# Performance work log

Measured on AMD Instinct MI355X. Metric: run time of the kernel, lower is better.

The kernel has to match this reference:

```python
import jax, jax.numpy as jnp
import numpy as np

D_MODEL = 2048
NUM_HEADS = 16
D_K = D_MODEL // NUM_HEADS  # 128
MAX_SEQ_LEN = 4096
THETA = 10000.0
BATCH = 2
SEQ = 2048


def _trunc_normal(key, shape, std):
    # approximate trunc_normal_(mean=0, std, a=-3std, b=3std)
    return jnp.clip(jax.random.normal(key, shape) * std, -3 * std, 3 * std)


def setup_inputs() -> dict:
    key = jax.random.key(0)
    k0, k1, k2, k3, k4 = jax.random.split(key, 5)
    std = 2.0 / (D_MODEL + D_MODEL) ** 0.5
    in_features = jax.random.normal(k0, (BATCH, SEQ, D_MODEL), dtype=jnp.float32)
    token_positions = jnp.arange(SEQ, dtype=jnp.int64 if jax.config.jax_enable_x64 else jnp.int32)
    wq = _trunc_normal(k1, (D_MODEL, D_MODEL), std)
    wk = _trunc_normal(k2, (D_MODEL, D_MODEL), std)
    wv = _trunc_normal(k3, (D_MODEL, D_MODEL), std)
    wo = _trunc_normal(k4, (D_MODEL, D_MODEL), std)
    return {"in_features": in_features, "token_positions": token_positions,
            "wq": wq, "wk": wk, "wv": wv, "wo": wo}


def _rope(x, token_positions):
    # x: [b, h, s, d_k]; token_positions: [s]
    freqs = 1.0 / THETA ** (jnp.arange(0, D_K, 2, dtype=jnp.float32) / D_K)  # [d_k/2]
    angles = token_positions.astype(jnp.float32)[:, None] * freqs[None, :]   # [s, d_k/2]
    sin = jnp.sin(angles)
    cos = jnp.cos(angles)
    x1 = x[..., ::2]
    x2 = x[..., 1::2]
    rot = jnp.stack([x1 * cos - x2 * sin, x1 * sin + x2 * cos], axis=-1)  # [b,h,s,d_k/2,2]
    return rot.reshape(x.shape)


def reference(in_features, token_positions, wq, wk, wv, wo):
    b, s, _ = in_features.shape
    # projections: weight is [d_out, d_in]
    q = jnp.einsum('oi,bsi->bso', wq, in_features)
    k = jnp.einsum('oi,bsi->bso', wk, in_features)
    v = jnp.einsum('oi,bsi->bso', wv, in_features)
    # split heads: [b, s, h*d] -> [b, h, s, d]
    def split(t):
        return t.reshape(b, s, NUM_HEADS, D_K).transpose(0, 2, 1, 3)
    q, k, v = split(q), split(k), split(v)
    q = _rope(q, token_positions)
    k = _rope(k, token_positions)
    scores = jnp.einsum('bhqd,bhkd->bhqk', q, k) / jnp.sqrt(jnp.float32(D_K))
    causal = jnp.tril(jnp.ones((s, s), dtype=bool))
    scores = jnp.where(causal, scores, -jnp.inf)
    attn = jax.nn.softmax(scores, axis=-1)
    out = jnp.einsum('bhqk,bhkd->bhqd', attn, v)
    out = out.transpose(0, 2, 1, 3).reshape(b, s, D_MODEL)
    return jnp.einsum('oi,bsi->bso', wo, out)
```

## Files before the change

kernel.cpp:

```cpp
#include <hip/hip_runtime.h>
#include <cstdint>

typedef unsigned short u16;
typedef __attribute__((ext_vector_type(8))) short short8;
typedef __attribute__((ext_vector_type(4))) float f32x4;
typedef __attribute__((ext_vector_type(16))) float f32x16;
typedef __attribute__((ext_vector_type(2))) unsigned int uint2v;

#define D_MODEL 2048
#define NHEAD   16
#define DK      128
#define SEQQ    2048
#define BATCH   2
#define MTOT    (BATCH*SEQQ)

#define FENCE() asm volatile("" ::: "memory")
#define BARRIER() do { FENCE(); __builtin_amdgcn_s_barrier(); FENCE(); } while (0)

__device__ __forceinline__ u16 f2b(float f) {
  union { float f; uint32_t u; } c; c.f = f;
  uint32_t u = c.u;
  u += 0x7fffu + ((u >> 16) & 1u);
  return (u16)(u >> 16);
}
__device__ __forceinline__ float b2f(u16 h) {
  union { uint32_t u; float f; } c; c.u = ((uint32_t)h) << 16;
  return c.f;
}

__device__ __forceinline__ void gload_lds16(const void* g, void* l) {
  __builtin_amdgcn_global_load_lds(
      (const __attribute__((address_space(1))) void*)(uintptr_t)g,
      (__attribute__((address_space(3))) void*)(uint32_t)(uintptr_t)l,
      16, 0, 0);
}

__global__ __launch_bounds__(256) void cvt_all(const float* __restrict__ x,
                                               const float* __restrict__ wq,
                                               const float* __restrict__ wk,
                                               const float* __restrict__ wv,
                                               const float* __restrict__ wo,
                                               u16* __restrict__ Xb,
                                               u16* __restrict__ Wqkv,
                                               u16* __restrict__ Wob) {
  int i = blockIdx.x * 256 + threadIdx.x;
  const float* src; u16* dst; int j;
  if (i < 2097152) {
    src = x; dst = Xb; j = i;
  } else {
    int t = i - 2097152;
    int w = t >> 20; j = t & 1048575;
    src = (w == 0) ? wq : (w == 1) ? wk : (w == 2) ? wv : wo;
    dst = (w < 3) ? (Wqkv + (size_t)w * 4194304) : Wob;
  }
  float4 v = ((const float4*)src)[j];
  union { u16 s[4]; uint64_t q; } o;
  o.s[0] = f2b(v.x); o.s[1] = f2b(v.y); o.s[2] = f2b(v.z); o.s[3] = f2b(v.w);
  ((uint64_t*)dst)[j] = o.q;
}

template<int MF, int NF, int MODE, int MAP>
__global__ __launch_bounds__(512) void gemmT(const u16* __restrict__ A,
                                             const u16* __restrict__ B,
                                             u16* __restrict__ Cq, u16* __restrict__ Ck,
                                             u16* __restrict__ Vt, float* __restrict__ Cf,
                                             int nbm, int cpx) {
  constexpr int BM = MF * 32;
  constexpr int BN = NF * 64;
  constexpr int AG = BM / 64;
  constexpr int BG = NF;
  __shared__ __align__(16) u16 As[2][BM * 64];
  __shared__ __align__(16) u16 Bs[2][BN * 64];
  const int tid = threadIdx.x;
  const int wave = tid >> 6, lane = tid & 63;
  const int l15 = lane & 15, l4 = lane >> 4;
  const int wr = wave >> 2, wc = wave & 3;
  int bm, bn;
  if (MAP == 1) {
    const int xcd = (int)blockIdx.x & 7;
    const int loc = (int)blockIdx.x >> 3;
    bm = ((loc >> 5) << 3) + (loc & 7);
    bn = xcd * 4 + ((loc >> 3) & 3);
  } else {
    const int wg = ((int)blockIdx.x & 7) * cpx + ((int)blockIdx.x >> 3);
    bm = wg % nbm; bn = wg / nbm;
  }
  const int row0 = bm * BM, col0 = bn * BN;

  const u16* asrc[AG]; const u16* bsrc[BG];
  {
    const int r = tid >> 3, c8 = tid & 7;
#pragma unroll
    for (int g = 0; g < AG; ++g) {
      int row = g * 64 + r;
      asrc[g] = A + (size_t)(row0 + row) * 2048 + ((c8 ^ (row & 7)) << 3);
    }
#pragma unroll
    for (int g = 0; g < BG; ++g) {
      int row = g * 64 + r;
      bsrc[g] = B + (size_t)(col0 + row) * 2048 + ((c8 ^ (row & 7)) << 3);
    }
  }
  const int ldst = tid * 8;

  int aoff[MF][2], boff[NF][2];
#pragma unroll
  for (int m = 0; m < MF; ++m) {
    int row = wr * (MF * 16) + m * 16 + l15;
#pragma unroll
    for (int ks = 0; ks < 2; ++ks)
      aoff[m][ks] = row * 64 + (((ks * 4 + l4) ^ (l15 & 7)) << 3);
  }
#pragma unroll
  for (int n = 0; n < NF; ++n) {
    int row = wc * (NF * 16) + n * 16 + l15;
#pragma unroll
    for (int ks = 0; ks < 2; ++ks)
      boff[n][ks] = row * 64 + (((ks * 4 + l4) ^ (l15 & 7)) << 3);
  }

  f32x4 acc[MF][NF] = {};

#pragma unroll
  for (int g = 0; g < AG; ++g) gload_lds16(asrc[g], &As[0][g * 4096 + ldst]);
#pragma unroll
  for (int g = 0; g < BG; ++g) gload_lds16(bsrc[g], &Bs[0][g * 4096 + ldst]);

  for (int t = 0; t < 32; ++t) {
    const int buf = t & 1;
    __syncthreads();
    if (t + 1 < 32) {
#pragma unroll
      for (int g = 0; g < AG; ++g) gload_lds16(asrc[g] + ((t + 1) << 6), &As[buf ^ 1][g * 4096 + ldst]);
#pragma unroll
      for (int g = 0; g < BG; ++g) gload_lds16(bsrc[g] + ((t + 1) << 6), &Bs[buf ^ 1][g * 4096 + ldst]);
    }
    short8 bfr[NF][2], afr[MF][2];
#pragma unroll
    for (int n = 0; n < NF; ++n)
#pragma unroll
      for (int ks = 0; ks < 2; ++ks)
        bfr[n][ks] = *(const short8*)&Bs[buf][boff[n][ks]];
#pragma unroll
    for (int m = 0; m < MF; ++m)
#pragma unroll
      for (int ks = 0; ks < 2; ++ks)
        afr[m][ks] = *(const short8*)&As[buf][aoff[m][ks]];
    __builtin_amdgcn_s_setprio(1);
#pragma unroll
    for (int ks = 0; ks < 2; ++ks)
#pragma unroll
      for (int n = 0; n < NF; ++n)
#pragma unroll
        for (int m = 0; m < MF; ++m)
          acc[m][n] = __builtin_amdgcn_mfma_f32_16x16x32_bf16(afr[m][ks], bfr[n][ks], acc[m][n], 0, 0, 0);
    __builtin_amdgcn_s_setprio(0);
  }

#pragma unroll
  for (int m = 0; m < MF; ++m) {
    const int row = row0 + wr * (MF * 16) + m * 16 + l4 * 4;
#pragma unroll
    for (int n = 0; n < NF; ++n) {
      const int col = col0 + wc * (NF * 16) + n * 16 + l15;
      if (MODE == 1) {
#pragma unroll
        for (int r = 0; r < 4; ++r)
          Cf[(size_t)(row + r) * 2048 + col] = acc[m][n][r];
      } else {
        const int region = col >> 11;
        const int col2 = col & 2047;
        if (region < 2) {
          u16* Cx = region ? Ck : Cq;
#pragma unroll
          for (int r = 0; r < 4; ++r)
            Cx[(size_t)(row + r) * 2048 + col2] = f2b(acc[m][n][r]);
        } else {
          union { u16 h4[4]; uint64_t q; } pk;
#pragma unroll
          for (int r = 0; r < 4; ++r) pk.h4[r] = f2b(acc[m][n][r]);
          const int bb = row >> 11, ss = row & 2047;
          const int hh = col2 >> 7, dd = col2 & 127;
          *(uint64_t*)&Vt[((size_t)((bb << 4) + hh) * 128 + dd) * 2048 + ss] = pk.q;
        }
      }
    }
  }
}

__global__ __launch_bounds__(256) void rope_qk(u16* __restrict__ Qb, u16* __restrict__ Kb,
                                               const int* __restrict__ pos) {
  int p = blockIdx.x * 256 + threadIdx.x;
  u16* X = (p >> 22) ? Kb : Qb;
  int pp = p & 4194303;
  int m = pp >> 10, j2 = pp & 1023;
  int h = j2 >> 6, j = j2 & 63;
  int s = m & (SEQQ - 1);
  float fp = (float)pos[s];
  float freq = exp2f((float)j * -0.20762050593046014f);
  float ang = fp * freq;
  float sn, cs;
  sincosf(ang, &sn, &cs);
  u16* px = X + (size_t)m * D_MODEL + h * DK + 2 * j;
  uint32_t pair = *(uint32_t*)px;
  float x1 = b2f((u16)(pair & 0xffff)), x2 = b2f((u16)(pair >> 16));
  u16 r1 = f2b(x1 * cs - x2 * sn);
  u16 r2 = f2b(x1 * sn + x2 * cs);
  *(uint32_t*)px = (uint32_t)r1 | ((uint32_t)r2 << 16);
}

__global__ __launch_bounds__(256) void attn_fwd(const u16* __restrict__ Q,
                                                const u16* __restrict__ Kg,
                                                const u16* __restrict__ Vt,
                                                u16* __restrict__ O) {
  __shared__ __align__(16) u16 Klds[2][64 * 128];
  __shared__ __align__(16) u16 Vlds[2][128 * 64];
  const int tid = threadIdx.x, wave = tid >> 6, lane = tid & 63;
  const int l31 = lane & 31, l5 = lane >> 5;
  const int bh = blockIdx.x;
  const int bxr = 15 - (int)blockIdx.y;
  const int b = bh >> 4, h = bh & 15;
  const int q0 = bxr * 128, qw = q0 + wave * 32;
  const float qscale = 0.1275174470974136f;

  short8 bq[8];
  {
    const u16* Qp = Q + (size_t)(b * SEQQ + qw + l31) * D_MODEL + h * DK + l5 * 8;
#pragma unroll
    for (int dt = 0; dt < 8; ++dt) {
      short8 raw = *(const short8*)(Qp + dt * 16);
#pragma unroll
      for (int j = 0; j < 8; ++j) raw[j] = (short)f2b(b2f((u16)raw[j]) * qscale);
      bq[dt] = raw;
    }
  }
  asm volatile("s_waitcnt vmcnt(0)" ::: "memory");

  f32x16 facc[4] = {};
  float mrun = -1e30f, lpart = 0.f;

  const u16* Kbase = Kg + (size_t)b * SEQQ * D_MODEL + h * DK;
  const u16* Vbase = Vt + (size_t)bh * DK * SEQQ;
  const u16* ksrc[4]; const u16* vsrc[4];
#pragma unroll
  for (int g = 0; g < 4; ++g) {
    int kr = g * 16 + (tid >> 4);
    int kc = ((tid & 15) * 8) ^ ((kr & 7) << 3);
    ksrc[g] = Kbase + (size_t)kr * D_MODEL + kc;
    int vr = g * 32 + (tid >> 3);
    int vc = ((tid & 7) * 8) ^ ((vr & 7) << 3);
    vsrc[g] = Vbase + (size_t)vr * SEQQ + vc;
  }
  const int dstoff = tid * 8;
  const int nkt = 2 * (bxr + 1);

#pragma unroll
  for (int g = 0; g < 4; ++g) { gload_lds16(ksrc[g], &Klds[0][g * 2048 + dstoff]); ksrc[g] += (size_t)64 * D_MODEL; }
#pragma unroll
  for (int g = 0; g < 4; ++g) { gload_lds16(vsrc[g], &Vlds[0][g * 2048 + dstoff]); vsrc[g] += 64; }

  for (int kt = 0; kt < nkt; ++kt) {
    const int k0 = kt * 64, cur = kt & 1;
    asm volatile("s_waitcnt vmcnt(0)" ::: "memory");
    BARRIER();
    if (kt + 1 < nkt) {
#pragma unroll
      for (int g = 0; g < 4; ++g) { gload_lds16(ksrc[g], &Klds[cur ^ 1][g * 2048 + dstoff]); ksrc[g] += (size_t)64 * D_MODEL; }
#pragma unroll
      for (int g = 0; g < 4; ++g) { gload_lds16(vsrc[g], &Vlds[cur ^ 1][g * 2048 + dstoff]); vsrc[g] += 64; }
    }
    if (k0 > qw + 31) continue;

    const u16* Kl = Klds[cur];
    const u16* Vl = Vlds[cur];

    f32x16 st0 = {}, st1 = {};
    __builtin_amdgcn_s_setprio(1);
#pragma unroll
    for (int dt = 0; dt < 8; ++dt) {
      const int ch = ((2 * dt + l5) ^ (l31 & 7)) * 8;
      short8 ak0 = *(const short8*)&Kl[l31 * 128 + ch];
      short8 ak1 = *(const short8*)&Kl[(32 + l31) * 128 + ch];
      st0 = __builtin_amdgcn_mfma_f32_32x32x16_bf16(ak0, bq[dt], st0, 0, 0, 0);
      st1 = __builtin_amdgcn_mfma_f32_32x32x16_bf16(ak1, bq[dt], st1, 0, 0, 0);
    }
    __builtin_amdgcn_s_setprio(0);

    if (k0 + 63 > qw) {
      const int qm = qw + l31 - k0 - 4 * l5;
#pragma unroll
      for (int r = 0; r < 16; ++r) {
        const int kc0 = (r & 3) + 8 * (r >> 2);
        st0[r] = (kc0 > qm) ? -1e30f : st0[r];
        st1[r] = (kc0 + 32 > qm) ? -1e30f : st1[r];
      }
    }

    float mx[8];
#pragma unroll
    for (int r = 0; r < 8; ++r) mx[r] = fmaxf(fmaxf(st0[r], st0[r + 8]), fmaxf(st1[r], st1[r + 8]));
    float m = fmaxf(fmaxf(fmaxf(mx[0], mx[1]), fmaxf(mx[2], mx[3])),
                    fmaxf(fmaxf(mx[4], mx[5]), fmaxf(mx[6], mx[7])));
    {
      uint2v sw = __builtin_amdgcn_permlane32_swap(__float_as_uint(m), __float_as_uint(m), false, false);
      m = fmaxf(__uint_as_float(sw.x), __uint_as_float(sw.y));
    }
    const float mn = fmaxf(mrun, m);
    const float al = exp2f(mrun - mn);
    mrun = mn;
    float ps = 0.f;
#pragma unroll
    for (int r = 0; r < 16; ++r) { float p = exp2f(st0[r] - mn); st0[r] = p; ps += p; }
#pragma unroll
    for (int r = 0; r < 16; ++r) { float p = exp2f(st1[r] - mn); st1[r] = p; ps += p; }
    lpart = lpart * al + ps;
#pragma unroll
    for (int db = 0; db < 4; ++db) facc[db] *= al;

    short8 pa[4];
#pragma unroll
    for (int ks2 = 0; ks2 < 2; ++ks2) {
#pragma unroll
      for (int t0 = 0; t0 < 2; ++t0) {
        uint32_t c0w0, c0w1, c1w0, c1w1;
        if (ks2 == 0) {
          asm("v_cvt_pk_bf16_f32 %0, %1, %2" : "=v"(c0w0) : "v"(st0[8 * t0 + 0]), "v"(st0[8 * t0 + 1]));
          asm("v_cvt_pk_bf16_f32 %0, %1, %2" : "=v"(c0w1) : "v"(st0[8 * t0 + 2]), "v"(st0[8 * t0 + 3]));
          asm("v_cvt_pk_bf16_f32 %0, %1, %2" : "=v"(c1w0) : "v"(st0[8 * t0 + 4]), "v"(st0[8 * t0 + 5]));
          asm("v_cvt_pk_bf16_f32 %0, %1, %2" : "=v"(c1w1) : "v"(st0[8 * t0 + 6]), "v"(st0[8 * t0 + 7]));
        } else {
          asm("v_cvt_pk_bf16_f32 %0, %1, %2" : "=v"(c0w0) : "v"(st1[8 * t0 + 0]), "v"(st1[8 * t0 + 1]));
          asm("v_cvt_pk_bf16_f32 %0, %1, %2" : "=v"(c0w1) : "v"(st1[8 * t0 + 2]), "v"(st1[8 * t0 + 3]));
          asm("v_cvt_pk_bf16_f32 %0, %1, %2" : "=v"(c1w0) : "v"(st1[8 * t0 + 4]), "v"(st1[8 * t0 + 5]));
          asm("v_cvt_pk_bf16_f32 %0, %1, %2" : "=v"(c1w1) : "v"(st1[8 * t0 + 6]), "v"(st1[8 * t0 + 7]));
        }
        uint2v s0 = __builtin_amdgcn_permlane32_swap(c0w0, c1w0, false, false);
        uint2v s1 = __builtin_amdgcn_permlane32_swap(c0w1, c1w1, false, false);
        union { uint32_t w[4]; short8 v; } u;
        u.w[0] = s0.x; u.w[1] = s1.x; u.w[2] = s0.y; u.w[3] = s1.y;
        pa[2 * ks2 + t0] = u.v;
      }
    }

    __builtin_amdgcn_s_setprio(1);
#pragma unroll
    for (int db = 0; db < 4; ++db) {
      const int row = 32 * db + l31;
#pragma unroll
      for (int t = 0; t < 4; ++t) {
        const int ch = ((2 * t + l5) ^ (l31 & 7)) * 8;
        short8 av = *(const short8*)&Vl[row * 64 + ch];
        facc[db] = __builtin_amdgcn_mfma_f32_32x32x16_bf16(av, pa[t], facc[db], 0, 0, 0);
      }
    }
    __builtin_amdgcn_s_setprio(0);
  }

  float inv;
  {
    uint2v sw = __builtin_amdgcn_permlane32_swap(__float_as_uint(lpart), __float_as_uint(lpart), false, false);
    inv = 1.0f / (__uint_as_float(sw.x) + __uint_as_float(sw.y));
  }
  u16* Op = O + (size_t)(b * SEQQ + qw + l31) * D_MODEL + h * DK;
#pragma unroll
  for (int db = 0; db < 4; ++db)
#pragma unroll
    for (int a = 0; a < 4; ++a) {
      union { u16 h4[4]; uint64_t q; } pk;
#pragma unroll
      for (int c = 0; c < 4; ++c) pk.h4[c] = f2b(facc[db][4 * a + c] * inv);
      *(uint64_t*)&Op[32 * db + 8 * a + 4 * l5] = pk.q;
    }
}

extern "C" void kernel_launch(void* const* d_in, const int* in_sizes, int n_in,
                              void* d_out, int out_size, void* d_ws, size_t ws_size,
                              hipStream_t stream) {
  const float* x   = (const float*)d_in[0];
  const int*   pos = (const int*)d_in[1];
  const float* wq  = (const float*)d_in[2];
  const float* wk  = (const float*)d_in[3];
  const float* wv  = (const float*)d_in[4];
  const float* wo  = (const float*)d_in[5];
  float* out = (float*)d_out;
  char* ws = (char*)d_ws;

  u16* Xb   = (u16*)(ws);
  u16* Wqkv = (u16*)(ws + (16u << 20));
  u16* Wob  = (u16*)(ws + (40u << 20));
  u16* Qb   = (u16*)(ws + (48u << 20));
  u16* Kb   = (u16*)(ws + (64u << 20));
  u16* Vt   = (u16*)(ws + (80u << 20));
  u16* AO   = Xb;

  cvt_all<<<24576, 256, 0, stream>>>(x, wq, wk, wv, wo, Xb, Wqkv, Wob);

  gemmT<4, 3, 0, 1><<<1024, 512, 0, stream>>>(Xb, Wqkv, Qb, Kb, Vt, nullptr, 32, 128);

  rope_qk<<<32768, 256, 0, stream>>>(Qb, Kb, pos);

  attn_fwd<<<dim3(32, 16), 256, 0, stream>>>(Qb, Kb, Vt, AO);

  gemmT<4, 4, 1, 0><<<256, 512, 0, stream>>>(AO, Wob, nullptr, nullptr, nullptr, out, 32, 32);
}
```

Before: 263.5 us.

## Fuse RoPE into QKV GEMM epilogue with precomputed sin/cos table

Removes the separate rope_qk kernel, which made a full read-modify-write pass over Q and K. RoPE is now applied in the QKV GEMM epilogue, using a DPP swap to get the partner element and a cos/sin table that cvt_all builds. Because the table reuses the Wo bf16 buffer region, the wo conversion moves to its own kernel launched after the QKV GEMM. The attention QK^T loop is also split into two independent accumulator chains to shorten MFMA dependency chains, and the PV loop order is swapped.

New measurement: 248.6 us. 5.6% less time.

```diff
diff --git a/kernel.cpp b/kernel.cpp
--- a/kernel.cpp
+++ b/kernel.cpp
@@ -39,24 +39,41 @@
                                                const float* __restrict__ wq,
                                                const float* __restrict__ wk,
                                                const float* __restrict__ wv,
-                                               const float* __restrict__ wo,
+                                               const int* __restrict__ pos,
                                                u16* __restrict__ Xb,
                                                u16* __restrict__ Wqkv,
-                                               u16* __restrict__ Wob) {
+                                               float2* __restrict__ Tab) {
   int i = blockIdx.x * 256 + threadIdx.x;
-  const float* src; u16* dst; int j;
-  if (i < 2097152) {
-    src = x; dst = Xb; j = i;
+  if (i < 5242880) {
+    const float* src; u16* dst; int j;
+    if (i < 2097152) { src = x; dst = Xb; j = i; }
+    else {
+      int t = i - 2097152;
+      int w = t >> 20; j = t & 1048575;
+      src = (w == 0) ? wq : (w == 1) ? wk : wv;
+      dst = Wqkv + (size_t)w * 4194304;
+    }
+    float4 v = ((const float4*)src)[j];
+    union { u16 s[4]; uint64_t q; } o;
+    o.s[0] = f2b(v.x); o.s[1] = f2b(v.y); o.s[2] = f2b(v.z); o.s[3] = f2b(v.w);
+    ((uint64_t*)dst)[j] = o.q;
   } else {
-    int t = i - 2097152;
-    int w = t >> 20; j = t & 1048575;
-    src = (w == 0) ? wq : (w == 1) ? wk : (w == 2) ? wv : wo;
-    dst = (w < 3) ? (Wqkv + (size_t)w * 4194304) : Wob;
-  }
-  float4 v = ((const float4*)src)[j];
+    int idx = i - 5242880;
+    int s = idx >> 6, j = idx & 63;
+    float ang = (float)pos[s] * exp2f((float)j * -0.20762050593046014f);
+    float sn, cs;
+    sincosf(ang, &sn, &cs);
+    Tab[idx] = make_float2(cs, sn);
+  }
+}
+
+__global__ __launch_bounds__(256) void cvt_wo(const float* __restrict__ wo,
+                                              u16* __restrict__ Wob) {
+  int i = blockIdx.x * 256 + threadIdx.x;
+  float4 v = ((const float4*)wo)[i];
   union { u16 s[4]; uint64_t q; } o;
   o.s[0] = f2b(v.x); o.s[1] = f2b(v.y); o.s[2] = f2b(v.z); o.s[3] = f2b(v.w);
-  ((uint64_t*)dst)[j] = o.q;
+  ((uint64_t*)Wob)[i] = o.q;
 }
 
 template<int MF, int NF, int MODE, int MAP>
@@ -64,6 +81,7 @@
                                              const u16* __restrict__ B,
                                              u16* __restrict__ Cq, u16* __restrict__ Ck,
                                              u16* __restrict__ Vt, float* __restrict__ Cf,
+                                             const float2* __restrict__ Tab,
                                              int nbm, int cpx) {
   constexpr int BM = MF * 32;
   constexpr int BN = NF * 64;
@@ -172,9 +190,16 @@
         const int col2 = col & 2047;
         if (region < 2) {
           u16* Cx = region ? Ck : Cq;
-#pragma unroll
-          for (int r = 0; r < 4; ++r)
-            Cx[(size_t)(row + r) * 2048 + col2] = f2b(acc[m][n][r]);
+          const float2* tp = Tab + (size_t)(row & 2047) * 64 + ((col2 & 127) >> 1);
+          const float sg = (col2 & 1) ? 1.0f : -1.0f;
+#pragma unroll
+          for (int r = 0; r < 4; ++r) {
+            float v = acc[m][n][r];
+            float p = __int_as_float(
+                __builtin_amdgcn_mov_dpp(__float_as_int(v), 0xB1, 0xF, 0xF, true));
+            float2 cs = tp[(size_t)r * 64];
+            Cx[(size_t)(row + r) * 2048 + col2] = f2b(fmaf(sg * p, cs.y, v * cs.x));
+          }
         } else {
           union { u16 h4[4]; uint64_t q; } pk;
 #pragma unroll
@@ -186,27 +211,6 @@
       }
     }
   }
-}
-
-__global__ __launch_bounds__(256) void rope_qk(u16* __restrict__ Qb, u16* __restrict__ Kb,
-                                               const int* __restrict__ pos) {
-  int p = blockIdx.x * 256 + threadIdx.x;
-  u16* X = (p >> 22) ? Kb : Qb;
-  int pp = p & 4194303;
-  int m = pp >> 10, j2 = pp & 1023;
-  int h = j2 >> 6, j = j2 & 63;
-  int s = m & (SEQQ - 1);
-  float fp = (float)pos[s];
-  float freq = exp2f((float)j * -0.20762050593046014f);
-  float ang = fp * freq;
-  float sn, cs;
-  sincosf(ang, &sn, &cs);
-  u16* px = X + (size_t)m * D_MODEL + h * DK + 2 * j;
-  uint32_t pair = *(uint32_t*)px;
-  float x1 = b2f((u16)(pair & 0xffff)), x2 = b2f((u16)(pair >> 16));
-  u16 r1 = f2b(x1 * cs - x2 * sn);
-  u16 r2 = f2b(x1 * sn + x2 * cs);
-  *(uint32_t*)px = (uint32_t)r1 | ((uint32_t)r2 << 16);
 }
 
 __global__ __launch_bounds__(256) void attn_fwd(const u16* __restrict__ Q,
@@ -274,17 +278,25 @@
     const u16* Kl = Klds[cur];
     const u16* Vl = Vlds[cur];
 
-    f32x16 st0 = {}, st1 = {};
+    f32x16 st0 = {}, st1 = {}, st0b = {}, st1b = {};
     __builtin_amdgcn_s_setprio(1);
 #pragma unroll
-    for (int dt = 0; dt < 8; ++dt) {
-      const int ch = ((2 * dt + l5) ^ (l31 & 7)) * 8;
-      short8 ak0 = *(const short8*)&Kl[l31 * 128 + ch];
-      short8 ak1 = *(const short8*)&Kl[(32 + l31) * 128 + ch];
-      st0 = __builtin_amdgcn_mfma_f32_32x32x16_bf16(ak0, bq[dt], st0, 0, 0, 0);
-      st1 = __builtin_amdgcn_mfma_f32_32x32x16_bf16(ak1, bq[dt], st1, 0, 0, 0);
+    for (int dtp = 0; dtp < 4; ++dtp) {
+      const int dt0 = 2 * dtp, dt1 = 2 * dtp + 1;
+      const int ch0 = ((2 * dt0 + l5) ^ (l31 & 7)) * 8;
+      const int ch1 = ((2 * dt1 + l5) ^ (l31 & 7)) * 8;
+      short8 ak00 = *(const short8*)&Kl[l31 * 128 + ch0];
+      short8 ak10 = *(const short8*)&Kl[(32 + l31) * 128 + ch0];
+      short8 ak01 = *(const short8*)&Kl[l31 * 128 + ch1];
+      short8 ak11 = *(const short8*)&Kl[(32 + l31) * 128 + ch1];
+      st0  = __builtin_amdgcn_mfma_f32_32x32x16_bf16(ak00, bq[dt0], st0, 0, 0, 0);
+      st1  = __builtin_amdgcn_mfma_f32_32x32x16_bf16(ak10, bq[dt0], st1, 0, 0, 0);
+      st0b = __builtin_amdgcn_mfma_f32_32x32x16_bf16(ak01, bq[dt1], st0b, 0, 0, 0);
+      st1b = __builtin_amdgcn_mfma_f32_32x32x16_bf16(ak11, bq[dt1], st1b, 0, 0, 0);
     }
     __builtin_amdgcn_s_setprio(0);
+    st0 += st0b;
+    st1 += st1b;
 
     if (k0 + 63 > qw) {
       const int qm = qw + l31 - k0 - 4 * l5;
@@ -344,10 +356,10 @@
 
     __builtin_amdgcn_s_setprio(1);
 #pragma unroll
-    for (int db = 0; db < 4; ++db) {
-      const int row = 32 * db + l31;
-#pragma unroll
-      for (int t = 0; t < 4; ++t) {
+    for (int t = 0; t < 4; ++t) {
+#pragma unroll
+      for (int db = 0; db < 4; ++db) {
+        const int row = 32 * db + l31;
         const int ch = ((2 * t + l5) ^ (l31 & 7)) * 8;
         short8 av = *(const short8*)&Vl[row * 64 + ch];
         facc[db] = __builtin_amdgcn_mfma_f32_32x32x16_bf16(av, pa[t], facc[db], 0, 0, 0);
@@ -388,18 +400,19 @@
   u16* Xb   = (u16*)(ws);
   u16* Wqkv = (u16*)(ws + (16u << 20));
   u16* Wob  = (u16*)(ws + (40u << 20));
+  float2* Tab = (float2*)(ws + (40u << 20));
   u16* Qb   = (u16*)(ws + (48u << 20));
   u16* Kb   = (u16*)(ws + (64u << 20));
   u16* Vt   = (u16*)(ws + (80u << 20));
   u16* AO   = Xb;
 
-  cvt_all<<<24576, 256, 0, stream>>>(x, wq, wk, wv, wo, Xb, Wqkv, Wob);
-
-  gemmT<4, 3, 0, 1><<<1024, 512, 0, stream>>>(Xb, Wqkv, Qb, Kb, Vt, nullptr, 32, 128);
-
-  rope_qk<<<32768, 256, 0, stream>>>(Qb, Kb, pos);
+  cvt_all<<<20992, 256, 0, stream>>>(x, wq, wk, wv, pos, Xb, Wqkv, Tab);
+
+  gemmT<4, 3, 0, 1><<<1024, 512, 0, stream>>>(Xb, Wqkv, Qb, Kb, Vt, nullptr, Tab, 32, 128);
+
+  cvt_wo<<<4096, 256, 0, stream>>>(wo, Wob);
 
   attn_fwd<<<dim3(32, 16), 256, 0, stream>>>(Qb, Kb, Vt, AO);
 
-  gemmT<4, 4, 1, 0><<<256, 512, 0, stream>>>(AO, Wob, nullptr, nullptr, nullptr, out, 32, 32);
-}
+  gemmT<4, 4, 1, 0><<<256, 512, 0, stream>>>(AO, Wob, nullptr, nullptr, nullptr, out, Tab, 32, 32);
+}
```
